# Kernel tuning notes

Measured on AMD Instinct MI355X. Metric: run time of the kernel, lower is better.

## Reference

```python
import jax, jax.numpy as jnp
import numpy as np
from jax import lax

B, L, LQ, D_IN, ET, H, INIT_EMBED = 16, 256, 64, 32, 128, 4, 8
DIM = 2 * D_IN          # attention value/feature dim (x concat mask)
ETK = ET // H           # per-head time-embedding dim


def _lin(key, fan_in, shape):
    b = 1.0 / np.sqrt(fan_in)
    return jax.random.uniform(key, shape, jnp.float32, -b, b)


def setup_inputs() -> dict:
    key = jax.random.key(0)
    ks = jax.random.split(key, 24)
    inp = {
        "x": jax.random.normal(ks[0], (B, L, D_IN), jnp.float32),
        "time_steps": jnp.sort(jax.random.uniform(ks[1], (B, L), jnp.float32), axis=-1),
        "mask": (jax.random.uniform(ks[2], (B, L, D_IN)) > 0.5).astype(jnp.float32),
        "query": jnp.linspace(0.0, 1.0, LQ, dtype=jnp.float32),
        # time embedding: Linear(1,1) and Linear(1, ET-1)
        "w_lin": _lin(ks[3], 1, (1,)), "b_lin": _lin(ks[4], 1, (1,)),
        "w_per": _lin(ks[5], 1, (ET - 1,)), "b_per": _lin(ks[6], 1, (ET - 1,)),
        # attention projections (stored as (in,out))
        "Wq": _lin(ks[7], ET, (ET, ET)), "bq": _lin(ks[8], ET, (ET,)),
        "Wk": _lin(ks[9], ET, (ET, ET)), "bk": _lin(ks[10], ET, (ET,)),
        "Wo": _lin(ks[11], H * DIM, (H * DIM, ET)), "bo": _lin(ks[12], H * DIM, (ET,)),
        # vanilla RNN (tanh)
        "W_ih": _lin(ks[13], ET, (ET, ET)), "b_ih": _lin(ks[14], ET, (ET,)),
        "W_hh": _lin(ks[15], ET, (ET, ET)), "b_hh": _lin(ks[16], ET, (ET,)),
        "r1_w": _lin(ks[17], ET, (ET, 128)), "r1_b": _lin(ks[17], ET, (128,)),
        "r2_w": _lin(ks[18], 128, (128, 128)), "r2_b": _lin(ks[18], 128, (128,)),
        "r3_w": _lin(ks[19], 128, (128, ET)), "r3_b": _lin(ks[19], 128, (ET,)),
        "r4_w": _lin(ks[20], ET, (ET, INIT_EMBED)), "r4_b": _lin(ks[20], ET, (INIT_EMBED,)),
    }
    return inp


def reference(x, time_steps, mask, query,
              w_lin, b_lin, w_per, b_per,
              Wq, bq, Wk, bk, Wo, bo,
              W_ih, b_ih, W_hh, b_hh,
              r1_w, r1_b, r2_w, r2_b, r3_w, r3_b, r4_w, r4_b):
    def time_embed(tt):  # (...,) -> (..., ET)
        tt = tt[..., None]
        return jnp.concatenate([tt * w_lin + b_lin,
                                jnp.sin(tt * w_per + b_per)], axis=-1)

    xc = jnp.concatenate([x, mask], axis=-1)          # (B,L,DIM) value
    m2 = jnp.concatenate([mask, mask], axis=-1)       # (B,L,DIM)

    kemb = time_embed(time_steps)                     # (B,L,ET)
    qemb = time_embed(query)                          # (LQ,ET)

    q = (qemb @ Wq + bq).reshape(LQ, H, ETK).transpose(1, 0, 2)       # (H,LQ,ETK)
    k = (kemb @ Wk + bk).reshape(B, L, H, ETK).transpose(0, 2, 1, 3)  # (B,H,L,ETK)

    scores = jnp.einsum('hqe,bhke->bhqk', q, k) / np.sqrt(ETK)        # (B,H,LQ,L)
    # per-feature mask broadcast: (B,H,LQ,L,DIM)
    s5 = jnp.where(m2[:, None, None, :, :] == 0, -1e9, scores[..., None])
    p = jax.nn.softmax(s5, axis=-2)                   # softmax over keys L
    att = jnp.einsum('bhqkd,bkd->bhqd', p, xc)        # (B,H,LQ,DIM)
    att = att.transpose(0, 2, 1, 3).reshape(B, LQ, H * DIM)
    out = att @ Wo + bo                               # (B,LQ,ET)

    # vanilla tanh RNN, return final hidden state
    def step(h, xt):
        h = jnp.tanh(xt @ W_ih + b_ih + h @ W_hh + b_hh)
        return h, None
    h0 = jnp.zeros((B, ET), out.dtype)
    hT, _ = lax.scan(step, h0, out.transpose(1, 0, 2))  # scan over LQ

    y = hT @ r1_w + r1_b
    y = y @ r2_w + r2_b
    y = y @ r3_w + r3_b
    y = y @ r4_w + r4_b                               # (B, INIT_EMBED)
    return y
```

## Files before the change

kernel.cpp:

```cpp
#include <hip/hip_runtime.h>
#include <hip/hip_bf16.h>

typedef __hip_bfloat16 bf16;
__device__ __forceinline__ float tof(bf16 v) { return __bfloat162float(v); }

#define NB 16
#define NL 256
#define NLQ 64
#define NDIN 32
#define NET 128
#define NH 4
#define NETK 32
#define NDIM 64
#define N_IN 26

struct CvtArgs {
  const void* src[N_IN];
  int cum[N_IN + 1];
};

__global__ __launch_bounds__(256) void k_cvt(CvtArgs a, const unsigned* __restrict__ qraw,
                                             float* __restrict__ dst, int total) {
  bool is_f32 = (qraw[0] == 0u);
  int g = blockIdx.x * 256 + threadIdx.x;
  if (g >= total) return;
  int s = 0;
  while (g >= a.cum[s + 1]) s++;
  int off = g - a.cum[s];
  float v;
  if (is_f32) v = ((const float*)a.src[s])[off];
  else        v = tof(((const bf16*)a.src[s])[off]);
  dst[g] = v;
}

__global__ __launch_bounds__(128) void k_embed_proj(
    const float* __restrict__ ts, const float* __restrict__ query,
    const float* __restrict__ w_lin, const float* __restrict__ b_lin,
    const float* __restrict__ w_per, const float* __restrict__ b_per,
    const float* __restrict__ Wk, const float* __restrict__ bk,
    const float* __restrict__ Wq, const float* __restrict__ bq,
    float* __restrict__ kproj, float* __restrict__ qproj) {
  __shared__ float emb[NET];
  int r = blockIdx.x;
  int j = threadIdx.x;
  bool isQ = (r >= NB * NL);
  float t = isQ ? query[r - NB * NL] : ts[r];
  float e;
  if (j == 0) e = t * w_lin[0] + b_lin[0];
  else        e = sinf(t * w_per[j - 1] + b_per[j - 1]);
  emb[j] = e;
  __syncthreads();
  const float* W = isQ ? Wq : Wk;
  float acc0 = isQ ? bq[j] : bk[j];
  float acc1 = 0.f, acc2 = 0.f, acc3 = 0.f;
#pragma unroll 8
  for (int i = 0; i < NET; i += 4) {
    acc0 += emb[i]     * W[(i)     * NET + j];
    acc1 += emb[i + 1] * W[(i + 1) * NET + j];
    acc2 += emb[i + 2] * W[(i + 2) * NET + j];
    acc3 += emb[i + 3] * W[(i + 3) * NET + j];
  }
  float acc = (acc0 + acc1) + (acc2 + acc3);
  if (isQ) qproj[(r - NB * NL) * NET + j] = acc;
  else     kproj[r * NET + j] = acc;
}

__global__ __launch_bounds__(256) void k_attn(
    const float* __restrict__ x, const float* __restrict__ mask,
    const float* __restrict__ qproj, const float* __restrict__ kproj,
    float* __restrict__ att) {
  const float SC = 0.17677669529663687f;
  int idx = blockIdx.x;
  int qg = idx & 7;
  int h  = (idx >> 3) & 3;
  int b  = idx >> 5;
  __shared__ float xs[NL * NDIN];
  __shared__ unsigned mb[NL];
  __shared__ float es[8 * NL];
  __shared__ float qs[8 * NETK];
  int t = threadIdx.x;

  {
    int qq = t >> 5, i = t & 31;
    qs[t] = qproj[(qg * 8 + qq) * NET + h * NETK + i];
  }
  {
    const float4* xb4 = (const float4*)(x + (size_t)b * NL * NDIN);
    float4* xs4 = (float4*)xs;
#pragma unroll
    for (int i = t; i < NL * NDIN / 4; i += 256) xs4[i] = xb4[i];
  }
  {
    const float4* mr4 = (const float4*)(mask + (size_t)(b * NL + t) * NDIN);
    unsigned bits = 0;
#pragma unroll
    for (int u = 0; u < 8; u++) {
      float4 m = mr4[u];
      bits |= (m.x != 0.f ? 1u : 0u) << (4 * u);
      bits |= (m.y != 0.f ? 1u : 0u) << (4 * u + 1);
      bits |= (m.z != 0.f ? 1u : 0u) << (4 * u + 2);
      bits |= (m.w != 0.f ? 1u : 0u) << (4 * u + 3);
    }
    mb[t] = bits;
  }
  float kr[NETK];
  {
    const float* kp = kproj + (size_t)(b * NL + t) * NET + h * NETK;
#pragma unroll
    for (int i = 0; i < NETK; i++) kr[i] = kp[i];
  }
  __syncthreads();
#pragma unroll
  for (int qq = 0; qq < 8; qq++) {
    float s0 = 0.f, s1 = 0.f;
#pragma unroll
    for (int i = 0; i < NETK; i += 2) {
      s0 += qs[qq * NETK + i]     * kr[i];
      s1 += qs[qq * NETK + i + 1] * kr[i + 1];
    }
    es[qq * NL + t] = __expf((s0 + s1) * SC);
  }
  __syncthreads();
  int qq = t >> 5, c = t & 31;
  float denom = 0.f, numx = 0.f, sumx = 0.f;
#pragma unroll 4
  for (int k = 0; k < NL; k++) {
    float e  = es[qq * NL + k];
    float mv = ((mb[k] >> c) & 1u) ? 1.f : 0.f;
    float xv = xs[k * NDIN + c];
    e *= mv;
    denom += e;
    numx  += e * xv;
    sumx  += xv;
  }
  float ax = (denom > 0.f) ? (numx / denom) : (sumx * (1.f / 256.f));
  float am = (denom > 0.f) ? 1.f : 0.f;
  int q = qg * 8 + qq;
  float* ao = att + (size_t)((b * NLQ + q) * NH + h) * NDIM;
  ao[c]      = ax;
  ao[32 + c] = am;
}

__global__ __launch_bounds__(128) void k_out_xw(
    const float* __restrict__ att,
    const float* __restrict__ Wo, const float* __restrict__ bo,
    const float* __restrict__ Wih, const float* __restrict__ bih,
    const float* __restrict__ bhh, float* __restrict__ XW) {
  int r = blockIdx.x;
  int j = threadIdx.x;
  __shared__ float arow[NH * NDIM];
  __shared__ float orow[NET];
  arow[j]       = att[(size_t)r * 256 + j];
  arow[j + 128] = att[(size_t)r * 256 + 128 + j];
  __syncthreads();
  float a0 = bo[j], a1 = 0.f, a2 = 0.f, a3 = 0.f;
#pragma unroll 8
  for (int u = 0; u < 256; u += 4) {
    a0 += arow[u]     * Wo[(u)     * NET + j];
    a1 += arow[u + 1] * Wo[(u + 1) * NET + j];
    a2 += arow[u + 2] * Wo[(u + 2) * NET + j];
    a3 += arow[u + 3] * Wo[(u + 3) * NET + j];
  }
  orow[j] = (a0 + a1) + (a2 + a3);
  __syncthreads();
  float b0 = bih[j] + bhh[j], b1 = 0.f, b2 = 0.f, b3 = 0.f;
#pragma unroll 8
  for (int e = 0; e < NET; e += 4) {
    b0 += orow[e]     * Wih[(e)     * NET + j];
    b1 += orow[e + 1] * Wih[(e + 1) * NET + j];
    b2 += orow[e + 2] * Wih[(e + 2) * NET + j];
    b3 += orow[e + 3] * Wih[(e + 3) * NET + j];
  }
  XW[(size_t)r * NET + j] = (b0 + b1) + (b2 + b3);
}

__global__ __launch_bounds__(128, 1) void k_rnn(
    const float* __restrict__ XW, const float* __restrict__ Whh,
    const float* __restrict__ r1w, const float* __restrict__ r1b,
    const float* __restrict__ r2w, const float* __restrict__ r2b,
    const float* __restrict__ r3w, const float* __restrict__ r3b,
    const float* __restrict__ r4w, const float* __restrict__ r4b,
    const unsigned* __restrict__ qraw, void* __restrict__ outv) {
  bool is_f32 = (qraw[0] == 0u);
  int b = blockIdx.x;
  int j = threadIdx.x;
  __shared__ float h[NET];
  __shared__ float tmp[NET];
  float w[NET];
#pragma unroll
  for (int i = 0; i < NET; i++) w[i] = Whh[i * NET + j];
  h[j] = 0.f;
  __syncthreads();
  for (int t = 0; t < NLQ; t++) {
    float acc = XW[(size_t)(b * NLQ + t) * NET + j];
    float a0 = 0.f, a1 = 0.f, a2 = 0.f, a3 = 0.f;
#pragma unroll
    for (int i = 0; i < NET; i += 4) {
      a0 += h[i]     * w[i];
      a1 += h[i + 1] * w[i + 1];
      a2 += h[i + 2] * w[i + 2];
      a3 += h[i + 3] * w[i + 3];
    }
    acc += (a0 + a1) + (a2 + a3);
    float hn = tanhf(acc);
    __syncthreads();
    h[j] = hn;
    __syncthreads();
  }
  {
    float a0 = r1b[j], a1 = 0.f, a2 = 0.f, a3 = 0.f;
#pragma unroll 8
    for (int i = 0; i < NET; i += 4) {
      a0 += h[i]     * r1w[(i)     * 128 + j];
      a1 += h[i + 1] * r1w[(i + 1) * 128 + j];
      a2 += h[i + 2] * r1w[(i + 2) * 128 + j];
      a3 += h[i + 3] * r1w[(i + 3) * 128 + j];
    }
    tmp[j] = (a0 + a1) + (a2 + a3);
  }
  __syncthreads();
  {
    float a0 = r2b[j], a1 = 0.f, a2 = 0.f, a3 = 0.f;
#pragma unroll 8
    for (int i = 0; i < 128; i += 4) {
      a0 += tmp[i]     * r2w[(i)     * 128 + j];
      a1 += tmp[i + 1] * r2w[(i + 1) * 128 + j];
      a2 += tmp[i + 2] * r2w[(i + 2) * 128 + j];
      a3 += tmp[i + 3] * r2w[(i + 3) * 128 + j];
    }
    float v = (a0 + a1) + (a2 + a3);
    __syncthreads();
    h[j] = v;
  }
  __syncthreads();
  {
    float a0 = r3b[j], a1 = 0.f, a2 = 0.f, a3 = 0.f;
#pragma unroll 8
    for (int i = 0; i < 128; i += 4) {
      a0 += h[i]     * r3w[(i)     * NET + j];
      a1 += h[i + 1] * r3w[(i + 1) * NET + j];
      a2 += h[i + 2] * r3w[(i + 2) * NET + j];
      a3 += h[i + 3] * r3w[(i + 3) * NET + j];
    }
    float v = (a0 + a1) + (a2 + a3);
    __syncthreads();
    tmp[j] = v;
  }
  __syncthreads();
  if (j < 8) {
    float y = r4b[j];
#pragma unroll 8
    for (int i = 0; i < NET; i++) y += tmp[i] * r4w[i * 8 + j];
    if (is_f32) ((float*)outv)[b * 8 + j] = y;
    else        ((bf16*)outv)[b * 8 + j] = __float2bfloat16(y);
  }
}

extern "C" void kernel_launch(void* const* d_in, const int* in_sizes, int n_in,
                              void* d_out, int out_size, void* d_ws, size_t ws_size,
                              hipStream_t stream) {
  CvtArgs a;
  int cum = 0;
  for (int i = 0; i < N_IN; i++) {
    a.src[i] = d_in[i];
    a.cum[i] = cum;
    cum += in_sizes[i];
  }
  a.cum[N_IN] = cum;
  int total = cum;
  int totalR = (total + 63) & ~63;

  float* ws = (float*)d_ws;
  float* F = ws;
  const float* x     = F + a.cum[0];
  const float* ts    = F + a.cum[1];
  const float* mask  = F + a.cum[2];
  const float* query = F + a.cum[3];
  const float* w_lin = F + a.cum[4];
  const float* b_lin = F + a.cum[5];
  const float* w_per = F + a.cum[6];
  const float* b_per = F + a.cum[7];
  const float* Wq    = F + a.cum[8];
  const float* bq    = F + a.cum[9];
  const float* Wk    = F + a.cum[10];
  const float* bk    = F + a.cum[11];
  const float* Wo    = F + a.cum[12];
  const float* bo    = F + a.cum[13];
  const float* Wih   = F + a.cum[14];
  const float* bih   = F + a.cum[15];
  const float* Whh   = F + a.cum[16];
  const float* bhh   = F + a.cum[17];
  const float* r1w   = F + a.cum[18];
  const float* r1b   = F + a.cum[19];
  const float* r2w   = F + a.cum[20];
  const float* r2b   = F + a.cum[21];
  const float* r3w   = F + a.cum[22];
  const float* r3b   = F + a.cum[23];
  const float* r4w   = F + a.cum[24];
  const float* r4b   = F + a.cum[25];

  float* qproj = ws + totalR;
  float* kproj = qproj + 8192;
  float* att   = kproj + 524288;
  float* XW    = att + 262144;

  const unsigned* qraw = (const unsigned*)d_in[3];

  k_cvt<<<(total + 255) / 256, 256, 0, stream>>>(a, qraw, F, total);
  k_embed_proj<<<NB * NL + NLQ, 128, 0, stream>>>(
      ts, query, w_lin, b_lin, w_per, b_per, Wk, bk, Wq, bq, kproj, qproj);
  k_attn<<<NB * NH * 8, 256, 0, stream>>>(x, mask, qproj, kproj, att);
  k_out_xw<<<NB * NLQ, 128, 0, stream>>>(att, Wo, bo, Wih, bih, bhh, XW);
  k_rnn<<<NB, 128, 0, stream>>>(XW, Whh, r1w, r1b, r2w, r2b, r3w, r3b,
                                r4w, r4b, qraw, (void*)d_out);
}
```

Baseline: 205.4 us.

## Split RNN hidden dot products across thread pairs with double-buffered state

The RNN kernel now uses 256 threads per batch row, with each pair of threads splitting the 128-term recurrent dot product and combining the halves through a lane shuffle. The hidden state is double-buffered in LDS, which cuts the two barriers per timestep to one. XW inputs are prefetched into registers, and tanh is replaced by a fast exp-based formula. The regressor layers use the same pair split, and the last layer uses a shuffle reduction. The aim is to shorten the serial 64-step critical path, at the cost of slightly different tanh precision.

```diff
diff --git a/kernel.cpp b/kernel.cpp
--- a/kernel.cpp
+++ b/kernel.cpp
@@ -174,7 +174,27 @@
   XW[(size_t)r * NET + j] = (b0 + b1) + (b2 + b3);
 }
 
-__global__ __launch_bounds__(128, 1) void k_rnn(
+__device__ __forceinline__ void layer128(const float* src_lds,
+                                         const float* __restrict__ W,
+                                         const float* __restrict__ bvec,
+                                         float* dst_lds, int j, int s) {
+  const float4* h4 = (const float4*)(src_lds + s * 64);
+  float a0 = 0.f, a1 = 0.f, a2 = 0.f, a3 = 0.f;
+#pragma unroll
+  for (int i = 0; i < 16; i++) {
+    float4 hv = h4[i];
+    int base = (s * 64 + 4 * i) * NET + j;
+    a0 += hv.x * W[base];
+    a1 += hv.y * W[base + NET];
+    a2 += hv.z * W[base + 2 * NET];
+    a3 += hv.w * W[base + 3 * NET];
+  }
+  float acc = (a0 + a1) + (a2 + a3);
+  acc += __shfl_xor(acc, 1, 64);
+  if (s == 0) dst_lds[j] = acc + bvec[j];
+}
+
+__global__ __launch_bounds__(256, 1) void k_rnn(
     const float* __restrict__ XW, const float* __restrict__ Whh,
     const float* __restrict__ r1w, const float* __restrict__ r1b,
     const float* __restrict__ r2w, const float* __restrict__ r2b,
@@ -183,76 +203,67 @@
     const unsigned* __restrict__ qraw, void* __restrict__ outv) {
   bool is_f32 = (qraw[0] == 0u);
   int b = blockIdx.x;
-  int j = threadIdx.x;
-  __shared__ float h[NET];
+  int tid = threadIdx.x;
+  int s = tid & 1;
+  int j = tid >> 1;
+  __shared__ float hb[2][NET];
   __shared__ float tmp[NET];
-  float w[NET];
-#pragma unroll
-  for (int i = 0; i < NET; i++) w[i] = Whh[i * NET + j];
-  h[j] = 0.f;
-  __syncthreads();
+
+  float w[64];
+#pragma unroll
+  for (int i = 0; i < 64; i++) w[i] = Whh[(s * 64 + i) * NET + j];
+  float xw[32];
+#pragma unroll
+  for (int u = 0; u < 32; u++)
+    xw[u] = XW[(size_t)(b * NLQ + 2 * u + s) * NET + j];
+
+  hb[0][tid & 127] = 0.f;
+  __syncthreads();
+
+#pragma unroll 2
   for (int t = 0; t < NLQ; t++) {
-    float acc = XW[(size_t)(b * NLQ + t) * NET + j];
+    const float4* h4 = (const float4*)&hb[t & 1][s * 64];
     float a0 = 0.f, a1 = 0.f, a2 = 0.f, a3 = 0.f;
 #pragma unroll
-    for (int i = 0; i < NET; i += 4) {
-      a0 += h[i]     * w[i];
-      a1 += h[i + 1] * w[i + 1];
-      a2 += h[i + 2] * w[i + 2];
-      a3 += h[i + 3] * w[i + 3];
-    }
-    acc += (a0 + a1) + (a2 + a3);
-    float hn = tanhf(acc);
+    for (int i = 0; i < 16; i++) {
+      float4 hv = h4[i];
+      a0 += hv.x * w[4 * i];
+      a1 += hv.y * w[4 * i + 1];
+      a2 += hv.z * w[4 * i + 2];
+      a3 += hv.w * w[4 * i + 3];
+    }
+    float acc = (a0 + a1) + (a2 + a3);
+    acc += __shfl_xor(acc, 1, 64);
+    if (s == (t & 1)) {
+      float z = acc + xw[t >> 1];
+      float e2 = __expf(2.f * z);
+      hb[(t + 1) & 1][j] = 1.f - 2.f / (e2 + 1.f);
+    }
     __syncthreads();
-    h[j] = hn;
-    __syncthreads();
-  }
-  {
-    float a0 = r1b[j], a1 = 0.f, a2 = 0.f, a3 = 0.f;
-#pragma unroll 8
-    for (int i = 0; i < NET; i += 4) {
-      a0 += h[i]     * r1w[(i)     * 128 + j];
-      a1 += h[i + 1] * r1w[(i + 1) * 128 + j];
-      a2 += h[i + 2] * r1w[(i + 2) * 128 + j];
-      a3 += h[i + 3] * r1w[(i + 3) * 128 + j];
-    }
-    tmp[j] = (a0 + a1) + (a2 + a3);
-  }
-  __syncthreads();
-  {
-    float a0 = r2b[j], a1 = 0.f, a2 = 0.f, a3 = 0.f;
-#pragma unroll 8
-    for (int i = 0; i < 128; i += 4) {
-      a0 += tmp[i]     * r2w[(i)     * 128 + j];
-      a1 += tmp[i + 1] * r2w[(i + 1) * 128 + j];
-      a2 += tmp[i + 2] * r2w[(i + 2) * 128 + j];
-      a3 += tmp[i + 3] * r2w[(i + 3) * 128 + j];
-    }
-    float v = (a0 + a1) + (a2 + a3);
-    __syncthreads();
-    h[j] = v;
-  }
-  __syncthreads();
-  {
-    float a0 = r3b[j], a1 = 0.f, a2 = 0.f, a3 = 0.f;
-#pragma unroll 8
-    for (int i = 0; i < 128; i += 4) {
-      a0 += h[i]     * r3w[(i)     * NET + j];
-      a1 += h[i + 1] * r3w[(i + 1) * NET + j];
-      a2 += h[i + 2] * r3w[(i + 2) * NET + j];
-      a3 += h[i + 3] * r3w[(i + 3) * NET + j];
-    }
-    float v = (a0 + a1) + (a2 + a3);
-    __syncthreads();
-    tmp[j] = v;
-  }
-  __syncthreads();
-  if (j < 8) {
-    float y = r4b[j];
-#pragma unroll 8
-    for (int i = 0; i < NET; i++) y += tmp[i] * r4w[i * 8 + j];
-    if (is_f32) ((float*)outv)[b * 8 + j] = y;
-    else        ((bf16*)outv)[b * 8 + j] = __float2bfloat16(y);
+  }
+
+  layer128(hb[0], r1w, r1b, tmp, j, s);
+  __syncthreads();
+  layer128(tmp, r2w, r2b, hb[1], j, s);
+  __syncthreads();
+  layer128(hb[1], r3w, r3b, hb[0], j, s);
+  __syncthreads();
+  if (tid < 64) {
+    int jj = tid >> 3, p = tid & 7;
+    float y = 0.f;
+#pragma unroll
+    for (int i = 0; i < 16; i++) {
+      int ii = p * 16 + i;
+      y += hb[0][ii] * r4w[ii * 8 + jj];
+    }
+    y += __shfl_xor(y, 1, 64);
+    y += __shfl_xor(y, 2, 64);
+    y += __shfl_xor(y, 4, 64);
+    if (p == 0) {
+      y += r4b[jj];
+      if (is_f32) ((float*)outv)[b * 8 + jj] = y;
+      else        ((bf16*)outv)[b * 8 + jj] = __float2bfloat16(y);
+    }
   }
 }
 
@@ -311,6 +322,6 @@
       ts, query, w_lin, b_lin, w_per, b_per, Wk, bk, Wq, bq, kproj, qproj);
   k_attn<<<NB * NH * 8, 256, 0, stream>>>(x, mask, qproj, kproj, att);
   k_out_xw<<<NB * NLQ, 128, 0, stream>>>(att, Wo, bo, Wih, bih, bhh, XW);
-  k_rnn<<<NB, 128, 0, stream>>>(XW, Whh, r1w, r1b, r2w, r2b, r3w, r3b,
+  k_rnn<<<NB, 256, 0, stream>>>(XW, Whh, r1w, r1b, r2w, r2b, r3w, r3b,
                                 r4w, r4b, qraw, (void*)d_out);
 }
```

After: 187.4 us. 8.7% less time.
